# Optimization experiments

Measured on AMD Instinct MI355X. Metric: run time of the kernel, lower is better.

## Reference

```python
import jax, jax.numpy as jnp
import numpy as np

N_NODES = 100000
N_EDGES = 800000
D = 96
BN_EPS = 1e-5
LEAKY_SLOPE = 0.05


def setup_inputs() -> dict:
    key = jax.random.key(0)
    ks = jax.random.split(key, 6)
    node_feat = jax.random.normal(ks[0], (N_NODES, D), dtype=jnp.float32)
    edge_index = jax.random.randint(ks[1], (2, N_EDGES), 0, N_NODES, dtype=jnp.int64)
    W1 = jax.random.normal(ks[2], (D, D), dtype=jnp.float32) / np.sqrt(D)
    b1 = jnp.zeros((D,), dtype=jnp.float32)
    W2 = jax.random.normal(ks[3], (D, D), dtype=jnp.float32) / np.sqrt(D)
    b2 = jnp.zeros((D,), dtype=jnp.float32)
    bn_gamma = jnp.ones((D,), dtype=jnp.float32)
    bn_beta = jnp.zeros((D,), dtype=jnp.float32)
    bn_mean = jnp.zeros((D,), dtype=jnp.float32)
    bn_var = jax.random.uniform(ks[4], (D,), dtype=jnp.float32, minval=0.5, maxval=1.5)
    return {"node_feat": node_feat, "edge_index": edge_index, "W1": W1, "b1": b1,
            "W2": W2, "b2": b2, "bn_gamma": bn_gamma, "bn_beta": bn_beta,
            "bn_mean": bn_mean, "bn_var": bn_var}


def _gcn_norm(edge_index, n_nodes, dtype):
    # add self-loops, symmetric normalization D^{-1/2} (A+I) D^{-1/2}
    loop = jnp.arange(n_nodes, dtype=edge_index.dtype)
    src = jnp.concatenate([edge_index[0], loop])
    dst = jnp.concatenate([edge_index[1], loop])
    deg = jax.ops.segment_sum(jnp.ones(src.shape, dtype=dtype), dst, num_segments=n_nodes)
    dinv = jnp.where(deg > 0, jax.lax.rsqrt(jnp.maximum(deg, 1e-12)), 0.0)
    norm = dinv[src] * dinv[dst]  # [E+N]
    return src, dst, norm


def _gcn_conv(x, W, b, src, dst, norm, n_nodes):
    h = x @ W                              # [N, d_out] dense GEMM
    msg = h[src] * norm[:, None]           # gather + scale, [E+N, d_out]
    agg = jax.ops.segment_sum(msg, dst, num_segments=n_nodes)  # scatter-add
    return agg + b


def reference(node_feat, edge_index, W1, b1, W2, b2, bn_gamma, bn_beta, bn_mean, bn_var):
    n = node_feat.shape[0]
    src, dst, norm = _gcn_norm(edge_index, n, node_feat.dtype)
    # layer 1: GCNConv -> LeakyReLU(0.05) -> BatchNorm1d (eval) -> dropout(eval = identity)
    x = _gcn_conv(node_feat, W1, b1, src, dst, norm, n)
    x = jnp.where(x >= 0, x, LEAKY_SLOPE * x)
    x = (x - bn_mean) * jax.lax.rsqrt(bn_var + BN_EPS) * bn_gamma + bn_beta
    # layer 2 (final): GCNConv only
    x = _gcn_conv(x, W2, b2, src, dst, norm, n)
    return x
```

## Files before the change

kernel.cpp:

```cpp
#include <hip/hip_runtime.h>

#define DF 96
#define BN_EPS 1e-5f
#define SLOPE 0.05f
#define LPN 6
#define GBLK 192
#define NPBG (GBLK / LPN)
#define XPAD 104

typedef __attribute__((ext_vector_type(8))) short bf16x8;
typedef __attribute__((ext_vector_type(4))) float f32x4;
typedef __attribute__((ext_vector_type(8))) unsigned short u16x8;

__device__ __forceinline__ unsigned short f2bf(float f) {
    unsigned u = __builtin_bit_cast(unsigned, f);
    return (unsigned short)((u + 0x7FFFu + ((u >> 16) & 1u)) >> 16);
}
__device__ __forceinline__ float bf2f(unsigned short h) {
    return __builtin_bit_cast(float, (unsigned)h << 16);
}

__global__ __launch_bounds__(256) void k_prep(const float* __restrict__ gamma,
                                              const float* __restrict__ beta,
                                              const float* __restrict__ mean,
                                              const float* __restrict__ var,
                                              float* __restrict__ bnscale,
                                              float* __restrict__ bnbias,
                                              const float* __restrict__ W1,
                                              const float* __restrict__ W2,
                                              unsigned short* __restrict__ Wt1,
                                              unsigned short* __restrict__ Wt2,
                                              int* __restrict__ cnt, int n) {
    int i = blockIdx.x * 256 + threadIdx.x;
    if (i < DF * DF) {
        int nn = i / DF, k = i - nn * DF;
        Wt1[i] = f2bf(W1[k * DF + nn]);
        Wt2[i] = f2bf(W2[k * DF + nn]);
    }
    if (i < DF) {
        float s = gamma[i] * rsqrtf(var[i] + BN_EPS);
        bnscale[i] = s;
        bnbias[i]  = beta[i] - mean[i] * s;
    }
    if (i < n) cnt[i] = 0;
}

__global__ __launch_bounds__(256) void k_countrank(const int* __restrict__ ei,
                                                   int* __restrict__ cnt,
                                                   int* __restrict__ rank, int E) {
    int i = blockIdx.x * 256 + threadIdx.x;
    int e = i * 2;
    if (e + 1 < E) {
        int2 d = *(const int2*)&ei[E + e];
        int r0 = atomicAdd(&cnt[d.x], 1);
        int r1 = atomicAdd(&cnt[d.y], 1);
        *(int2*)&rank[e] = make_int2(r0, r1);
    } else if (e < E) {
        rank[e] = atomicAdd(&cnt[ei[E + e]], 1);
    }
}

__global__ __launch_bounds__(256) void k_scan1(const int* __restrict__ cnt,
                                               int* __restrict__ rowptr,
                                               int* __restrict__ bsum, int n) {
    __shared__ int sh[256];
    int t = threadIdx.x;
    int i = blockIdx.x * 256 + t;
    int x = (i < n) ? cnt[i] : 0;
    sh[t] = x;
    __syncthreads();
#pragma unroll
    for (int off = 1; off < 256; off <<= 1) {
        int v = (t >= off) ? sh[t - off] : 0;
        __syncthreads();
        sh[t] += v;
        __syncthreads();
    }
    if (i < n) rowptr[i] = sh[t] - x;
    if (t == 255) bsum[blockIdx.x] = sh[255];
}

__global__ __launch_bounds__(512) void k_scan23(int* __restrict__ rowptr,
                                                const int* __restrict__ bsum,
                                                const int* __restrict__ cnt,
                                                float* __restrict__ dinv,
                                                int n, int E, int nb) {
    __shared__ int sh[512];
    __shared__ int sbex[512];
    const int t = threadIdx.x;
    int x = (t < nb) ? bsum[t] : 0;
    sh[t] = x;
    __syncthreads();
#pragma unroll
    for (int off = 1; off < 512; off <<= 1) {
        int v = (t >= off) ? sh[t - off] : 0;
        __syncthreads();
        sh[t] += v;
        __syncthreads();
    }
    sbex[t] = sh[t] - x;
    __syncthreads();

    const int i = blockIdx.x * 512 + t;
    if (i < n) {
        rowptr[i] = rowptr[i] + sbex[i >> 8];
        dinv[i]   = rsqrtf((float)cnt[i] + 1.0f);
    }
    if (i == 0) rowptr[n] = E;
}

__device__ __forceinline__ void gemm1_body(int bid, int tid, const float* __restrict__ in,
                                           const unsigned short* __restrict__ Wt,
                                           const float* __restrict__ dinv,
                                           unsigned short* __restrict__ outb, int n) {
    const int wave = tid >> 6;
    const int lane = tid & 63;
    const int l16  = lane & 15;
    const int quad = lane >> 4;
    const int rowbase = bid * 64 + wave * 16;
    const int m = rowbase + l16;
    const bool valid = (m < n);

    bf16x8 bfrag[6][3];
#pragma unroll
    for (int nt = 0; nt < 6; ++nt)
#pragma unroll
        for (int ks = 0; ks < 3; ++ks)
            bfrag[nt][ks] = *(const bf16x8*)&Wt[(nt * 16 + l16) * DF + ks * 32 + quad * 8];

    const float* rowp = in + (size_t)m * DF;
    float4 ra[3][2];
#pragma unroll
    for (int ks = 0; ks < 3; ++ks) {
        if (valid) {
            ra[ks][0] = *(const float4*)&rowp[ks * 32 + quad * 8];
            ra[ks][1] = *(const float4*)&rowp[ks * 32 + quad * 8 + 4];
        } else {
            ra[ks][0] = make_float4(0.f, 0.f, 0.f, 0.f);
            ra[ks][1] = make_float4(0.f, 0.f, 0.f, 0.f);
        }
    }
    bf16x8 afrag[3];
#pragma unroll
    for (int ks = 0; ks < 3; ++ks) {
        const float* a0 = (const float*)&ra[ks][0];
        const float* a1 = (const float*)&ra[ks][1];
        bf16x8 f;
#pragma unroll
        for (int j = 0; j < 4; ++j) {
            f[j]     = (short)f2bf(a0[j]);
            f[j + 4] = (short)f2bf(a1[j]);
        }
        afrag[ks] = f;
    }

    f32x4 acc[6] = {};
#pragma unroll
    for (int ks = 0; ks < 3; ++ks)
#pragma unroll
        for (int nt = 0; nt < 6; ++nt)
            acc[nt] = __builtin_amdgcn_mfma_f32_16x16x32_bf16(afrag[ks], bfrag[nt][ks],
                                                              acc[nt], 0, 0, 0);

#pragma unroll
    for (int reg = 0; reg < 4; ++reg) {
        const int r = rowbase + quad * 4 + reg;
        if (r < n) {
            const float dv = dinv[r];
#pragma unroll
            for (int nt = 0; nt < 6; ++nt)
                outb[(size_t)r * DF + nt * 16 + l16] = f2bf(acc[nt][reg] * dv);
        }
    }
}

__device__ __forceinline__ void fill_body(int bid, int tid, const int* __restrict__ ei,
                                          const int* __restrict__ rowptr,
                                          const int* __restrict__ rank,
                                          int* __restrict__ csr, int E) {
    int e = bid * 256 + tid;
    if (e < E) {
        int src = ei[e];
        int dst = ei[E + e];
        csr[rowptr[dst] + rank[e]] = src;
    }
}

__global__ __launch_bounds__(256) void k_gemm1_fill(const float* __restrict__ in,
                                                    const unsigned short* __restrict__ Wt1,
                                                    const float* __restrict__ dinv,
                                                    unsigned short* __restrict__ bufA,
                                                    int n, int gb,
                                                    const int* __restrict__ ei,
                                                    const int* __restrict__ rowptr,
                                                    const int* __restrict__ rank,
                                                    int* __restrict__ csr, int E) {
    const int b = blockIdx.x;
    if (b < gb) gemm1_body(b, threadIdx.x, in, Wt1, dinv, bufA, n);
    else        fill_body(b - gb, threadIdx.x, ei, rowptr, rank, csr, E);
}

__global__ __launch_bounds__(GBLK) void k_gather0_gemm2(const int* __restrict__ rowptr,
                                                        const int* __restrict__ csr,
                                                        const unsigned short* __restrict__ hs,
                                                        const float* __restrict__ dinv,
                                                        const float* __restrict__ b1,
                                                        const float* __restrict__ bnscale,
                                                        const float* __restrict__ bnbias,
                                                        const unsigned short* __restrict__ Wt2,
                                                        unsigned short* __restrict__ outb,
                                                        int n) {
    __shared__ unsigned short sx[NPBG * XPAD];
    const int t  = threadIdx.x;
    const int vl = t / LPN;
    const int q  = t % LPN;
    const int v  = blockIdx.x * NPBG + vl;

    if (v < n) {
        float acc[16];
        {
            const unsigned short* p0 = &hs[(size_t)v * DF + q * 16];
            const u16x8 h0 = *(const u16x8*)p0;
            const u16x8 h1 = *(const u16x8*)(p0 + 8);
#pragma unroll
            for (int i = 0; i < 8; ++i) {
                acc[i]     = bf2f(h0[i]);
                acc[8 + i] = bf2f(h1[i]);
            }
        }
        const int e1 = rowptr[v + 1];
        int e = rowptr[v];
        for (; e + 8 <= e1; e += 8) {
            int s[8];
#pragma unroll
            for (int u = 0; u < 8; ++u) s[u] = csr[e + u];
            u16x8 ma[8], mb[8];
#pragma unroll
            for (int u = 0; u < 8; ++u) {
                const unsigned short* p = &hs[(size_t)s[u] * DF + q * 16];
                ma[u] = *(const u16x8*)p;
                mb[u] = *(const u16x8*)(p + 8);
            }
#pragma unroll
            for (int u = 0; u < 8; ++u)
#pragma unroll
                for (int i = 0; i < 8; ++i) {
                    acc[i]     += bf2f(ma[u][i]);
                    acc[8 + i] += bf2f(mb[u][i]);
                }
        }
        for (; e + 4 <= e1; e += 4) {
            int s[4];
#pragma unroll
            for (int u = 0; u < 4; ++u) s[u] = csr[e + u];
            u16x8 ma[4], mb[4];
#pragma unroll
            for (int u = 0; u < 4; ++u) {
                const unsigned short* p = &hs[(size_t)s[u] * DF + q * 16];
                ma[u] = *(const u16x8*)p;
                mb[u] = *(const u16x8*)(p + 8);
            }
#pragma unroll
            for (int u = 0; u < 4; ++u)
#pragma unroll
                for (int i = 0; i < 8; ++i) {
                    acc[i]     += bf2f(ma[u][i]);
                    acc[8 + i] += bf2f(mb[u][i]);
                }
        }
        for (; e < e1; ++e) {
            const unsigned short* p = &hs[(size_t)csr[e] * DF + q * 16];
            const u16x8 m0 = *(const u16x8*)p;
            const u16x8 m1 = *(const u16x8*)(p + 8);
#pragma unroll
            for (int i = 0; i < 8; ++i) {
                acc[i]     += bf2f(m0[i]);
                acc[8 + i] += bf2f(m1[i]);
            }
        }

        const float dv = dinv[v];
        float bl[16], sc[16], bi[16];
#pragma unroll
        for (int j = 0; j < 4; ++j) {
            *(float4*)&bl[j * 4] = *(const float4*)&b1[q * 16 + j * 4];
            *(float4*)&sc[j * 4] = *(const float4*)&bnscale[q * 16 + j * 4];
            *(float4*)&bi[j * 4] = *(const float4*)&bnbias[q * 16 + j * 4];
        }
        u16x8 o0, o1;
#pragma unroll
        for (int i = 0; i < 8; ++i) {
            float x = __builtin_fmaf(dv, acc[i], bl[i]);
            x = (x >= 0.f) ? x : SLOPE * x;
            o0[i] = f2bf(__builtin_fmaf(x, sc[i], bi[i]));
            float y = __builtin_fmaf(dv, acc[8 + i], bl[8 + i]);
            y = (y >= 0.f) ? y : SLOPE * y;
            o1[i] = f2bf(__builtin_fmaf(y, sc[8 + i], bi[8 + i]));
        }
        *(u16x8*)&sx[vl * XPAD + q * 16]     = o0;
        *(u16x8*)&sx[vl * XPAD + q * 16 + 8] = o1;
    }
    __syncthreads();

    if (t < 128) {
        const int wave = t >> 6;
        const int l16  = t & 15;
        const int quad = (t >> 4) & 3;
        bf16x8 afrag[3];
#pragma unroll
        for (int ks = 0; ks < 3; ++ks)
            afrag[ks] = *(const bf16x8*)&sx[(wave * 16 + l16) * XPAD + ks * 32 + quad * 8];

        bf16x8 bfrag[6][3];
#pragma unroll
        for (int nt = 0; nt < 6; ++nt)
#pragma unroll
            for (int ks = 0; ks < 3; ++ks)
                bfrag[nt][ks] = *(const bf16x8*)&Wt2[(nt * 16 + l16) * DF + ks * 32 + quad * 8];

        f32x4 acc2[6] = {};
#pragma unroll
        for (int ks = 0; ks < 3; ++ks)
#pragma unroll
            for (int nt = 0; nt < 6; ++nt)
                acc2[nt] = __builtin_amdgcn_mfma_f32_16x16x32_bf16(afrag[ks], bfrag[nt][ks],
                                                                   acc2[nt], 0, 0, 0);

        const int rowbase = blockIdx.x * NPBG + wave * 16;
#pragma unroll
        for (int reg = 0; reg < 4; ++reg) {
            const int r = rowbase + quad * 4 + reg;
            if (r < n) {
                const float dv = dinv[r];
#pragma unroll
                for (int nt = 0; nt < 6; ++nt)
                    outb[(size_t)r * DF + nt * 16 + l16] = f2bf(acc2[nt][reg] * dv);
            }
        }
    }
}

__global__ __launch_bounds__(GBLK) void k_gather_final(const int* __restrict__ rowptr,
                                                       const int* __restrict__ csr,
                                                       const unsigned short* __restrict__ hs,
                                                       const float* __restrict__ dinv,
                                                       const float* __restrict__ b2,
                                                       float* __restrict__ outp, int n) {
    const int t = threadIdx.x;
    const int v = blockIdx.x * NPBG + t / LPN;
    const int q = t % LPN;
    if (v >= n) return;

    float acc[16];
    {
        const unsigned short* p0 = &hs[(size_t)v * DF + q * 16];
        const u16x8 h0 = *(const u16x8*)p0;
        const u16x8 h1 = *(const u16x8*)(p0 + 8);
#pragma unroll
        for (int i = 0; i < 8; ++i) {
            acc[i]     = bf2f(h0[i]);
            acc[8 + i] = bf2f(h1[i]);
        }
    }
    const int e1 = rowptr[v + 1];
    int e = rowptr[v];
    for (; e + 8 <= e1; e += 8) {
        int s[8];
#pragma unroll
        for (int u = 0; u < 8; ++u) s[u] = csr[e + u];
        u16x8 ma[8], mb[8];
#pragma unroll
        for (int u = 0; u < 8; ++u) {
            const unsigned short* p = &hs[(size_t)s[u] * DF + q * 16];
            ma[u] = *(const u16x8*)p;
            mb[u] = *(const u16x8*)(p + 8);
        }
#pragma unroll
        for (int u = 0; u < 8; ++u)
#pragma unroll
            for (int i = 0; i < 8; ++i) {
                acc[i]     += bf2f(ma[u][i]);
                acc[8 + i] += bf2f(mb[u][i]);
            }
    }
    for (; e + 4 <= e1; e += 4) {
        int s[4];
#pragma unroll
        for (int u = 0; u < 4; ++u) s[u] = csr[e + u];
        u16x8 ma[4], mb[4];
#pragma unroll
        for (int u = 0; u < 4; ++u) {
            const unsigned short* p = &hs[(size_t)s[u] * DF + q * 16];
            ma[u] = *(const u16x8*)p;
            mb[u] = *(const u16x8*)(p + 8);
        }
#pragma unroll
        for (int u = 0; u < 4; ++u)
#pragma unroll
            for (int i = 0; i < 8; ++i) {
                acc[i]     += bf2f(ma[u][i]);
                acc[8 + i] += bf2f(mb[u][i]);
            }
    }
    for (; e < e1; ++e) {
        const unsigned short* p = &hs[(size_t)csr[e] * DF + q * 16];
        const u16x8 m0 = *(const u16x8*)p;
        const u16x8 m1 = *(const u16x8*)(p + 8);
#pragma unroll
        for (int i = 0; i < 8; ++i) {
            acc[i]     += bf2f(m0[i]);
            acc[8 + i] += bf2f(m1[i]);
        }
    }

    const float dv = dinv[v];
    float bb[16];
#pragma unroll
    for (int j = 0; j < 4; ++j)
        *(float4*)&bb[j * 4] = *(const float4*)&b2[q * 16 + j * 4];

    float* op = (float*)outp + (size_t)v * DF + q * 16;
#pragma unroll
    for (int j = 0; j < 4; ++j) {
        float4 o;
        o.x = __builtin_fmaf(acc[j * 4 + 0], dv, bb[j * 4 + 0]);
        o.y = __builtin_fmaf(acc[j * 4 + 1], dv, bb[j * 4 + 1]);
        o.z = __builtin_fmaf(acc[j * 4 + 2], dv, bb[j * 4 + 2]);
        o.w = __builtin_fmaf(acc[j * 4 + 3], dv, bb[j * 4 + 3]);
        *(float4*)(op + j * 4) = o;
    }
}

extern "C" void kernel_launch(void* const* d_in, const int* in_sizes, int n_in,
                              void* d_out, int out_size, void* d_ws, size_t ws_size,
                              hipStream_t stream) {
    const float* node_feat = (const float*)d_in[0];
    const int*   ei        = (const int*)d_in[1];
    const float* W1        = (const float*)d_in[2];
    const float* b1        = (const float*)d_in[3];
    const float* W2        = (const float*)d_in[4];
    const float* b2        = (const float*)d_in[5];
    const float* gamma     = (const float*)d_in[6];
    const float* beta      = (const float*)d_in[7];
    const float* mean      = (const float*)d_in[8];
    const float* var       = (const float*)d_in[9];

    const int n  = in_sizes[0] / DF;
    const int E  = in_sizes[1] / 2;
    const int nb = (n + 255) / 256;

    char* base = (char*)d_ws;
    size_t off = 0;
    auto alloc = [&](size_t bytes) { void* p = base + off; off = (off + bytes + 15) & ~(size_t)15; return p; };
    int*   cnt     = (int*)alloc(sizeof(int) * n);
    int*   rowptr  = (int*)alloc(sizeof(int) * (n + 1));
    int*   bsum    = (int*)alloc(sizeof(int) * 512);
    float* dinv    = (float*)alloc(sizeof(float) * n);
    float* bnscale = (float*)alloc(sizeof(float) * DF);
    float* bnbias  = (float*)alloc(sizeof(float) * DF);
    unsigned short* Wt1 = (unsigned short*)alloc(sizeof(short) * DF * DF);
    unsigned short* Wt2 = (unsigned short*)alloc(sizeof(short) * DF * DF);
    int*   rank    = (int*)alloc(sizeof(int) * E);
    int*   csr     = (int*)alloc(sizeof(int) * E);
    unsigned short* bufA = (unsigned short*)alloc(sizeof(short) * (size_t)n * DF);
    unsigned short* bufB = (unsigned short*)alloc(sizeof(short) * (size_t)n * DF);
    float* out     = (float*)d_out;

    k_prep<<<nb, 256, 0, stream>>>(gamma, beta, mean, var, bnscale, bnbias,
                                   W1, W2, Wt1, Wt2, cnt, n);
    k_countrank<<<(E / 2 + 255) / 256, 256, 0, stream>>>(ei, cnt, rank, E);
    k_scan1<<<nb, 256, 0, stream>>>(cnt, rowptr, bsum, n);
    k_scan23<<<(n + 511) / 512, 512, 0, stream>>>(rowptr, bsum, cnt, dinv, n, E, nb);

    const int gb = (n + 63) / 64;
    const int fb = (E + 255) / 256;
    const int gg = (n + NPBG - 1) / NPBG;

    k_gemm1_fill<<<gb + fb, 256, 0, stream>>>(node_feat, Wt1, dinv, bufA, n, gb,
                                              ei, rowptr, rank, csr, E);
    k_gather0_gemm2<<<gg, GBLK, 0, stream>>>(rowptr, csr, bufA, dinv, b1, bnscale,
                                             bnbias, Wt2, bufB, n);
    k_gather_final<<<gg, GBLK, 0, stream>>>(rowptr, csr, bufB, dinv, b2, out, n);
}
```

Measured before the change: 249.9 us.

## Fuse degree count with GEMM1 and apply source dinv during gather

The GEMM1 stage no longer scales rows by the source dinv, so it no longer depends on the scan and can share a launch with the edge-count atomics. The CSR fill becomes its own kernel. Both gather kernels now load dinv[src] per edge and apply it with an FMA, and the self term is scaled by dinv[v]. The count kernel handles four edges per thread. The intent is to overlap the GEMM with the atomic counting and shorten the dependency chain. The cost is an extra random dinv load per edge in both gathers.

```diff
diff --git a/kernel.cpp b/kernel.cpp
--- a/kernel.cpp
+++ b/kernel.cpp
@@ -45,19 +45,97 @@
     if (i < n) cnt[i] = 0;
 }
 
-__global__ __launch_bounds__(256) void k_countrank(const int* __restrict__ ei,
-                                                   int* __restrict__ cnt,
-                                                   int* __restrict__ rank, int E) {
-    int i = blockIdx.x * 256 + threadIdx.x;
-    int e = i * 2;
-    if (e + 1 < E) {
-        int2 d = *(const int2*)&ei[E + e];
+__device__ __forceinline__ void gemm1_body(int bid, int tid, const float* __restrict__ in,
+                                           const unsigned short* __restrict__ Wt,
+                                           unsigned short* __restrict__ outb, int n) {
+    const int wave = tid >> 6;
+    const int lane = tid & 63;
+    const int l16  = lane & 15;
+    const int quad = lane >> 4;
+    const int rowbase = bid * 64 + wave * 16;
+    const int m = rowbase + l16;
+    const bool valid = (m < n);
+
+    bf16x8 bfrag[6][3];
+#pragma unroll
+    for (int nt = 0; nt < 6; ++nt)
+#pragma unroll
+        for (int ks = 0; ks < 3; ++ks)
+            bfrag[nt][ks] = *(const bf16x8*)&Wt[(nt * 16 + l16) * DF + ks * 32 + quad * 8];
+
+    const float* rowp = in + (size_t)m * DF;
+    float4 ra[3][2];
+#pragma unroll
+    for (int ks = 0; ks < 3; ++ks) {
+        if (valid) {
+            ra[ks][0] = *(const float4*)&rowp[ks * 32 + quad * 8];
+            ra[ks][1] = *(const float4*)&rowp[ks * 32 + quad * 8 + 4];
+        } else {
+            ra[ks][0] = make_float4(0.f, 0.f, 0.f, 0.f);
+            ra[ks][1] = make_float4(0.f, 0.f, 0.f, 0.f);
+        }
+    }
+    bf16x8 afrag[3];
+#pragma unroll
+    for (int ks = 0; ks < 3; ++ks) {
+        const float* a0 = (const float*)&ra[ks][0];
+        const float* a1 = (const float*)&ra[ks][1];
+        bf16x8 f;
+#pragma unroll
+        for (int j = 0; j < 4; ++j) {
+            f[j]     = (short)f2bf(a0[j]);
+            f[j + 4] = (short)f2bf(a1[j]);
+        }
+        afrag[ks] = f;
+    }
+
+    f32x4 acc[6] = {};
+#pragma unroll
+    for (int ks = 0; ks < 3; ++ks)
+#pragma unroll
+        for (int nt = 0; nt < 6; ++nt)
+            acc[nt] = __builtin_amdgcn_mfma_f32_16x16x32_bf16(afrag[ks], bfrag[nt][ks],
+                                                              acc[nt], 0, 0, 0);
+
+#pragma unroll
+    for (int reg = 0; reg < 4; ++reg) {
+        const int r = rowbase + quad * 4 + reg;
+        if (r < n) {
+#pragma unroll
+            for (int nt = 0; nt < 6; ++nt)
+                outb[(size_t)r * DF + nt * 16 + l16] = f2bf(acc[nt][reg]);
+        }
+    }
+}
+
+__device__ __forceinline__ void count_body(int bid, int tid, const int* __restrict__ ei,
+                                           int* __restrict__ cnt,
+                                           int* __restrict__ rank, int E) {
+    int i = bid * 256 + tid;
+    int e = i * 4;
+    if (e + 3 < E) {
+        int4 d = *(const int4*)&ei[E + e];
         int r0 = atomicAdd(&cnt[d.x], 1);
         int r1 = atomicAdd(&cnt[d.y], 1);
-        *(int2*)&rank[e] = make_int2(r0, r1);
-    } else if (e < E) {
-        rank[e] = atomicAdd(&cnt[ei[E + e]], 1);
-    }
+        int r2 = atomicAdd(&cnt[d.z], 1);
+        int r3 = atomicAdd(&cnt[d.w], 1);
+        *(int4*)&rank[e] = make_int4(r0, r1, r2, r3);
+    } else {
+        for (; e < E; ++e) rank[e] = atomicAdd(&cnt[ei[E + e]], 1);
+    }
+}
+
+__global__ __launch_bounds__(256) void k_count_gemm1(const int* __restrict__ ei,
+                                                     int* __restrict__ cnt,
+                                                     int* __restrict__ rank, int E,
+                                                     int cb,
+                                                     const float* __restrict__ in,
+                                                     const unsigned short* __restrict__ Wt1,
+                                                     unsigned short* __restrict__ bufA,
+                                                     int n) {
+    const int b = blockIdx.x;
+    if (b < cb) count_body(b, threadIdx.x, ei, cnt, rank, E);
+    else        gemm1_body(b - cb, threadIdx.x, in, Wt1, bufA, n);
 }
 
 __global__ __launch_bounds__(256) void k_scan1(const int* __restrict__ cnt,
@@ -109,95 +187,16 @@
     if (i == 0) rowptr[n] = E;
 }
 
-__device__ __forceinline__ void gemm1_body(int bid, int tid, const float* __restrict__ in,
-                                           const unsigned short* __restrict__ Wt,
-                                           const float* __restrict__ dinv,
-                                           unsigned short* __restrict__ outb, int n) {
-    const int wave = tid >> 6;
-    const int lane = tid & 63;
-    const int l16  = lane & 15;
-    const int quad = lane >> 4;
-    const int rowbase = bid * 64 + wave * 16;
-    const int m = rowbase + l16;
-    const bool valid = (m < n);
-
-    bf16x8 bfrag[6][3];
-#pragma unroll
-    for (int nt = 0; nt < 6; ++nt)
-#pragma unroll
-        for (int ks = 0; ks < 3; ++ks)
-            bfrag[nt][ks] = *(const bf16x8*)&Wt[(nt * 16 + l16) * DF + ks * 32 + quad * 8];
-
-    const float* rowp = in + (size_t)m * DF;
-    float4 ra[3][2];
-#pragma unroll
-    for (int ks = 0; ks < 3; ++ks) {
-        if (valid) {
-            ra[ks][0] = *(const float4*)&rowp[ks * 32 + quad * 8];
-            ra[ks][1] = *(const float4*)&rowp[ks * 32 + quad * 8 + 4];
-        } else {
-            ra[ks][0] = make_float4(0.f, 0.f, 0.f, 0.f);
-            ra[ks][1] = make_float4(0.f, 0.f, 0.f, 0.f);
-        }
-    }
-    bf16x8 afrag[3];
-#pragma unroll
-    for (int ks = 0; ks < 3; ++ks) {
-        const float* a0 = (const float*)&ra[ks][0];
-        const float* a1 = (const float*)&ra[ks][1];
-        bf16x8 f;
-#pragma unroll
-        for (int j = 0; j < 4; ++j) {
-            f[j]     = (short)f2bf(a0[j]);
-            f[j + 4] = (short)f2bf(a1[j]);
-        }
-        afrag[ks] = f;
-    }
-
-    f32x4 acc[6] = {};
-#pragma unroll
-    for (int ks = 0; ks < 3; ++ks)
-#pragma unroll
-        for (int nt = 0; nt < 6; ++nt)
-            acc[nt] = __builtin_amdgcn_mfma_f32_16x16x32_bf16(afrag[ks], bfrag[nt][ks],
-                                                              acc[nt], 0, 0, 0);
-
-#pragma unroll
-    for (int reg = 0; reg < 4; ++reg) {
-        const int r = rowbase + quad * 4 + reg;
-        if (r < n) {
-            const float dv = dinv[r];
-#pragma unroll
-            for (int nt = 0; nt < 6; ++nt)
-                outb[(size_t)r * DF + nt * 16 + l16] = f2bf(acc[nt][reg] * dv);
-        }
-    }
-}
-
-__device__ __forceinline__ void fill_body(int bid, int tid, const int* __restrict__ ei,
-                                          const int* __restrict__ rowptr,
-                                          const int* __restrict__ rank,
-                                          int* __restrict__ csr, int E) {
-    int e = bid * 256 + tid;
+__global__ __launch_bounds__(256) void k_fill(const int* __restrict__ ei,
+                                              const int* __restrict__ rowptr,
+                                              const int* __restrict__ rank,
+                                              int* __restrict__ csr, int E) {
+    int e = blockIdx.x * 256 + threadIdx.x;
     if (e < E) {
         int src = ei[e];
         int dst = ei[E + e];
         csr[rowptr[dst] + rank[e]] = src;
     }
-}
-
-__global__ __launch_bounds__(256) void k_gemm1_fill(const float* __restrict__ in,
-                                                    const unsigned short* __restrict__ Wt1,
-                                                    const float* __restrict__ dinv,
-                                                    unsigned short* __restrict__ bufA,
-                                                    int n, int gb,
-                                                    const int* __restrict__ ei,
-                                                    const int* __restrict__ rowptr,
-                                                    const int* __restrict__ rank,
-                                                    int* __restrict__ csr, int E) {
-    const int b = blockIdx.x;
-    if (b < gb) gemm1_body(b, threadIdx.x, in, Wt1, dinv, bufA, n);
-    else        fill_body(b - gb, threadIdx.x, ei, rowptr, rank, csr, E);
 }
 
 __global__ __launch_bounds__(GBLK) void k_gather0_gemm2(const int* __restrict__ rowptr,
@@ -217,6 +216,7 @@
     const int v  = blockIdx.x * NPBG + vl;
 
     if (v < n) {
+        const float dv = dinv[v];
         float acc[16];
         {
             const unsigned short* p0 = &hs[(size_t)v * DF + q * 16];
@@ -224,8 +224,8 @@
             const u16x8 h1 = *(const u16x8*)(p0 + 8);
 #pragma unroll
             for (int i = 0; i < 8; ++i) {
-                acc[i]     = bf2f(h0[i]);
-                acc[8 + i] = bf2f(h1[i]);
+                acc[i]     = dv * bf2f(h0[i]);
+                acc[8 + i] = dv * bf2f(h1[i]);
             }
         }
         const int e1 = rowptr[v + 1];
@@ -234,9 +234,11 @@
             int s[8];
 #pragma unroll
             for (int u = 0; u < 8; ++u) s[u] = csr[e + u];
+            float ds[8];
             u16x8 ma[8], mb[8];
 #pragma unroll
             for (int u = 0; u < 8; ++u) {
+                ds[u] = dinv[s[u]];
                 const unsigned short* p = &hs[(size_t)s[u] * DF + q * 16];
                 ma[u] = *(const u16x8*)p;
                 mb[u] = *(const u16x8*)(p + 8);
@@ -245,17 +247,19 @@
             for (int u = 0; u < 8; ++u)
 #pragma unroll
                 for (int i = 0; i < 8; ++i) {
-                    acc[i]     += bf2f(ma[u][i]);
-                    acc[8 + i] += bf2f(mb[u][i]);
+                    acc[i]     = __builtin_fmaf(ds[u], bf2f(ma[u][i]), acc[i]);
+                    acc[8 + i] = __builtin_fmaf(ds[u], bf2f(mb[u][i]), acc[8 + i]);
                 }
         }
         for (; e + 4 <= e1; e += 4) {
             int s[4];
 #pragma unroll
             for (int u = 0; u < 4; ++u) s[u] = csr[e + u];
+            float ds[4];
             u16x8 ma[4], mb[4];
 #pragma unroll
             for (int u = 0; u < 4; ++u) {
+                ds[u] = dinv[s[u]];
                 const unsigned short* p = &hs[(size_t)s[u] * DF + q * 16];
                 ma[u] = *(const u16x8*)p;
                 mb[u] = *(const u16x8*)(p + 8);
@@ -264,22 +268,23 @@
             for (int u = 0; u < 4; ++u)
 #pragma unroll
                 for (int i = 0; i < 8; ++i) {
-                    acc[i]     += bf2f(ma[u][i]);
-                    acc[8 + i] += bf2f(mb[u][i]);
+                    acc[i]     = __builtin_fmaf(ds[u], bf2f(ma[u][i]), acc[i]);
+                    acc[8 + i] = __builtin_fmaf(ds[u], bf2f(mb[u][i]), acc[8 + i]);
                 }
         }
         for (; e < e1; ++e) {
-            const unsigned short* p = &hs[(size_t)csr[e] * DF + q * 16];
+            const int s = csr[e];
+            const float dse = dinv[s];
+            const unsigned short* p = &hs[(size_t)s * DF + q * 16];
             const u16x8 m0 = *(const u16x8*)p;
             const u16x8 m1 = *(const u16x8*)(p + 8);
 #pragma unroll
             for (int i = 0; i < 8; ++i) {
-                acc[i]     += bf2f(m0[i]);
-                acc[8 + i] += bf2f(m1[i]);
-            }
-        }
-
-        const float dv = dinv[v];
+                acc[i]     = __builtin_fmaf(dse, bf2f(m0[i]), acc[i]);
+                acc[8 + i] = __builtin_fmaf(dse, bf2f(m1[i]), acc[8 + i]);
+            }
+        }
+
         float bl[16], sc[16], bi[16];
 #pragma unroll
         for (int j = 0; j < 4; ++j) {
@@ -331,10 +336,9 @@
         for (int reg = 0; reg < 4; ++reg) {
             const int r = rowbase + quad * 4 + reg;
             if (r < n) {
-                const float dv = dinv[r];
 #pragma unroll
                 for (int nt = 0; nt < 6; ++nt)
-                    outb[(size_t)r * DF + nt * 16 + l16] = f2bf(acc2[nt][reg] * dv);
+                    outb[(size_t)r * DF + nt * 16 + l16] = f2bf(acc2[nt][reg]);
             }
         }
     }
@@ -351,6 +355,7 @@
     const int q = t % LPN;
     if (v >= n) return;
 
+    const float dv = dinv[v];
     float acc[16];
     {
         const unsigned short* p0 = &hs[(size_t)v * DF + q * 16];
@@ -358,8 +363,8 @@
         const u16x8 h1 = *(const u16x8*)(p0 + 8);
 #pragma unroll
         for (int i = 0; i < 8; ++i) {
-            acc[i]     = bf2f(h0[i]);
-            acc[8 + i] = bf2f(h1[i]);
+            acc[i]     = dv * bf2f(h0[i]);
+            acc[8 + i] = dv * bf2f(h1[i]);
         }
     }
     const int e1 = rowptr[v + 1];
@@ -368,9 +373,11 @@
         int s[8];
 #pragma unroll
         for (int u = 0; u < 8; ++u) s[u] = csr[e + u];
+        float ds[8];
         u16x8 ma[8], mb[8];
 #pragma unroll
         for (int u = 0; u < 8; ++u) {
+            ds[u] = dinv[s[u]];
             const unsigned short* p = &hs[(size_t)s[u] * DF + q * 16];
             ma[u] = *(const u16x8*)p;
             mb[u] = *(const u16x8*)(p + 8);
@@ -379,17 +386,19 @@
         for (int u = 0; u < 8; ++u)
 #pragma unroll
             for (int i = 0; i < 8; ++i) {
-                acc[i]     += bf2f(ma[u][i]);
-                acc[8 + i] += bf2f(mb[u][i]);
+                acc[i]     = __builtin_fmaf(ds[u], bf2f(ma[u][i]), acc[i]);
+                acc[8 + i] = __builtin_fmaf(ds[u], bf2f(mb[u][i]), acc[8 + i]);
             }
     }
     for (; e + 4 <= e1; e += 4) {
         int s[4];
 #pragma unroll
         for (int u = 0; u < 4; ++u) s[u] = csr[e + u];
+        float ds[4];
         u16x8 ma[4], mb[4];
 #pragma unroll
         for (int u = 0; u < 4; ++u) {
+            ds[u] = dinv[s[u]];
             const unsigned short* p = &hs[(size_t)s[u] * DF + q * 16];
             ma[u] = *(const u16x8*)p;
             mb[u] = *(const u16x8*)(p + 8);
@@ -398,22 +407,23 @@
         for (int u = 0; u < 4; ++u)
 #pragma unroll
             for (int i = 0; i < 8; ++i) {
-                acc[i]     += bf2f(ma[u][i]);
-                acc[8 + i] += bf2f(mb[u][i]);
+                acc[i]     = __builtin_fmaf(ds[u], bf2f(ma[u][i]), acc[i]);
+                acc[8 + i] = __builtin_fmaf(ds[u], bf2f(mb[u][i]), acc[8 + i]);
             }
     }
     for (; e < e1; ++e) {
-        const unsigned short* p = &hs[(size_t)csr[e] * DF + q * 16];
+        const int s = csr[e];
+        const float dse = dinv[s];
+        const unsigned short* p = &hs[(size_t)s * DF + q * 16];
         const u16x8 m0 = *(const u16x8*)p;
         const u16x8 m1 = *(const u16x8*)(p + 8);
 #pragma unroll
         for (int i = 0; i < 8; ++i) {
-            acc[i]     += bf2f(m0[i]);
-            acc[8 + i] += bf2f(m1[i]);
-        }
-    }
-
-    const float dv = dinv[v];
+            acc[i]     = __builtin_fmaf(dse, bf2f(m0[i]), acc[i]);
+            acc[8 + i] = __builtin_fmaf(dse, bf2f(m1[i]), acc[8 + i]);
+        }
+    }
+
     float bb[16];
 #pragma unroll
     for (int j = 0; j < 4; ++j)
@@ -466,18 +476,18 @@
     unsigned short* bufB = (unsigned short*)alloc(sizeof(short) * (size_t)n * DF);
     float* out     = (float*)d_out;
 
-    k_prep<<<nb, 256, 0, stream>>>(gamma, beta, mean, var, bnscale, bnbias,
-                                   W1, W2, Wt1, Wt2, cnt, n);
-    k_countrank<<<(E / 2 + 255) / 256, 256, 0, stream>>>(ei, cnt, rank, E);
-    k_scan1<<<nb, 256, 0, stream>>>(cnt, rowptr, bsum, n);
-    k_scan23<<<(n + 511) / 512, 512, 0, stream>>>(rowptr, bsum, cnt, dinv, n, E, nb);
-
+    const int cb = (E + 1023) / 1024;
     const int gb = (n + 63) / 64;
     const int fb = (E + 255) / 256;
     const int gg = (n + NPBG - 1) / NPBG;
 
-    k_gemm1_fill<<<gb + fb, 256, 0, stream>>>(node_feat, Wt1, dinv, bufA, n, gb,
-                                              ei, rowptr, rank, csr, E);
+    k_prep<<<nb, 256, 0, stream>>>(gamma, beta, mean, var, bnscale, bnbias,
+                                   W1, W2, Wt1, Wt2, cnt, n);
+    k_count_gemm1<<<cb + gb, 256, 0, stream>>>(ei, cnt, rank, E, cb,
+                                               node_feat, Wt1, bufA, n);
+    k_scan1<<<nb, 256, 0, stream>>>(cnt, rowptr, bsum, n);
+    k_scan23<<<(n + 511) / 512, 512, 0, stream>>>(rowptr, bsum, cnt, dinv, n, E, nb);
+    k_fill<<<fb, 256, 0, stream>>>(ei, rowptr, rank, csr, E);
     k_gather0_gemm2<<<gg, GBLK, 0, stream>>>(rowptr, csr, bufA, dinv, b1, bnscale,
                                              bnbias, Wt2, bufB, n);
     k_gather_final<<<gg, GBLK, 0, stream>>>(rowptr, csr, bufB, dinv, b2, out, n);
```

After: 260.0 us. 4.0% more time.
